# Kernel optimization log

Measured on AMD Instinct MI355X. Metric: run time of the kernel, lower is better.

## Reference

```python
import jax, jax.numpy as jnp
import numpy as np

B, N, K, D = 16, 8192, 20, 64  # batch, points, neighbors, feature dim
LN_EPS = 1e-5


def setup_inputs() -> dict:
    key = jax.random.key(0)
    k1, k2, k3 = jax.random.split(key, 3)
    x = jax.random.normal(k1, (B, N, D), dtype=jnp.float32)
    neighbor_ind = jax.random.randint(k2, (B, N, K), 0, N)
    # torch Linear(2D -> D, bias=False): weight shape (out=D, in=2D), y = feat @ W.T
    W = jax.random.normal(k3, (D, 2 * D), dtype=jnp.float32) * (1.0 / np.sqrt(2 * D))
    gamma = jnp.ones((D,), jnp.float32)
    beta = jnp.zeros((D,), jnp.float32)
    return {"x": x, "neighbor_ind": neighbor_ind, "W": W, "gamma": gamma, "beta": beta}


def reference(x, neighbor_ind, W, gamma, beta):
    # route(): gather neighbor features and build [neighbor - center, center]
    neighbor_x = jax.vmap(lambda xb, ib: xb[ib])(x, neighbor_ind)        # (b, n, k, d)
    center = x[:, :, None, :]                                            # (b, n, 1, d)
    feat = jnp.concatenate(
        [neighbor_x - center, jnp.broadcast_to(center, neighbor_x.shape)], axis=-1
    )                                                                    # (b, n, k, 2d)
    # per-edge Linear (bias=False), then max over k neighbors
    h = jnp.einsum('bnke,oe->bnko', feat, W)                             # (b, n, k, d)
    h = h.max(axis=2)                                                    # (b, n, d)
    # LayerNorm over last dim, then exact GELU
    mu = h.mean(axis=-1, keepdims=True)
    var = jnp.mean((h - mu) ** 2, axis=-1, keepdims=True)
    hn = (h - mu) * jax.lax.rsqrt(var + LN_EPS) * gamma + beta
    return jax.nn.gelu(hn, approximate=False)
```

## Files before the change

### kernel.cpp

```cpp
#include <hip/hip_runtime.h>
#include <math.h>

#define B_ 16
#define N_ 8192
#define K_ 20
#define NPTS (B_ * N_)

typedef __attribute__((ext_vector_type(4))) float f4;
typedef __attribute__((ext_vector_type(8))) short s8;

__device__ __forceinline__ short f2bf(float f) {
    union { float f; unsigned u; } v; v.f = f;
    return (short)((v.u + 0x7FFFu + ((v.u >> 16) & 1u)) >> 16);
}

__device__ __forceinline__ f4 bf4_to_f4(ushort4 v) {
    f4 r;
    r.x = __uint_as_float((unsigned)v.x << 16);
    r.y = __uint_as_float((unsigned)v.y << 16);
    r.z = __uint_as_float((unsigned)v.z << 16);
    r.w = __uint_as_float((unsigned)v.w << 16);
    return r;
}

__global__ __launch_bounds__(256) void prep_kernel(const float* __restrict__ W,
                                                   unsigned short* __restrict__ Wg) {
    const int i = blockIdx.x * 256 + threadIdx.x;
    const int j = i >> 6, d = i & 63;
    const float v = (j < 64) ? W[j * 128 + d]
                             : (W[(j - 64) * 128 + 64 + d] - W[(j - 64) * 128 + d]);
    Wg[i] = (unsigned short)f2bf(v);
}

__global__ __launch_bounds__(256) void proj_kernel(const float* __restrict__ x,
                                                   const unsigned short* __restrict__ Wg,
                                                   unsigned short* __restrict__ Y1,
                                                   float* __restrict__ Bs) {
    __shared__ unsigned short Wl[128 * 72];
    const int t = threadIdx.x;

    for (int i = t; i < 1024; i += 256) {
        int4 v = ((const int4*)Wg)[i];
        *((int4*)((char*)Wl + (i >> 3) * 144 + (i & 7) * 16)) = v;
    }
    __syncthreads();

    const int lane = t & 63;
    const int wv = t >> 6;
    const int m = lane & 15;
    const int q = lane >> 4;
    const int rbase = blockIdx.x * 64 + wv * 16;

    const float* xr = x + (size_t)(rbase + m) * 64 + q * 8;
    f4 x0 = *(const f4*)(xr);
    f4 x1 = *(const f4*)(xr + 4);
    f4 x2 = *(const f4*)(xr + 32);
    f4 x3 = *(const f4*)(xr + 36);
    s8 A0, A1;
    A0[0]=f2bf(x0.x); A0[1]=f2bf(x0.y); A0[2]=f2bf(x0.z); A0[3]=f2bf(x0.w);
    A0[4]=f2bf(x1.x); A0[5]=f2bf(x1.y); A0[6]=f2bf(x1.z); A0[7]=f2bf(x1.w);
    A1[0]=f2bf(x2.x); A1[1]=f2bf(x2.y); A1[2]=f2bf(x2.z); A1[3]=f2bf(x2.w);
    A1[4]=f2bf(x3.x); A1[5]=f2bf(x3.y); A1[6]=f2bf(x3.z); A1[7]=f2bf(x3.w);

    f4 acc[8];
#pragma unroll
    for (int tt = 0; tt < 8; ++tt) acc[tt] = (f4)0.f;

#pragma unroll
    for (int s = 0; s < 2; ++s) {
        const s8 A = s ? A1 : A0;
#pragma unroll
        for (int tt = 0; tt < 8; ++tt) {
            s8 b = *(const s8*)((const char*)Wl + (16 * tt + m) * 144 + s * 64 + q * 16);
            acc[tt] = __builtin_amdgcn_mfma_f32_16x16x32_bf16(A, b, acc[tt], 0, 0, 0);
        }
    }

    const int orow = rbase + q * 4;
#pragma unroll
    for (int tt = 0; tt < 4; ++tt) {
#pragma unroll
        for (int j = 0; j < 4; ++j)
            Y1[(size_t)(orow + j) * 64 + 16 * tt + m] = (unsigned short)f2bf(acc[tt][j]);
    }
#pragma unroll
    for (int tt = 4; tt < 8; ++tt) {
#pragma unroll
        for (int j = 0; j < 4; ++j)
            Bs[(size_t)(orow + j) * 64 + 16 * (tt - 4) + m] = acc[tt][j];
    }
}

__global__ __launch_bounds__(256) void gather_kernel(const unsigned short* __restrict__ Y1,
                                                     const float* __restrict__ Bs,
                                                     const int* __restrict__ ind,
                                                     const float* __restrict__ gamma,
                                                     const float* __restrict__ beta,
                                                     float* __restrict__ out) {
    const int lane = threadIdx.x & 63;
    const int wave = threadIdx.x >> 6;
    const int sub = lane & 15;
    const int q = lane >> 4;
    const int bi = blockIdx.x;
    const int bt = bi & 15;
    const int jj = bi >> 4;
    const int p = bt * N_ + jj * 16 + wave * 4 + q;
    const int bbase = bt * N_ * 64;

    int idxs[K_];
    const int4* ip = (const int4*)&ind[p * K_];
#pragma unroll
    for (int v = 0; v < 5; ++v) {
        int4 iv = ip[v];
        idxs[4 * v + 0] = iv.x; idxs[4 * v + 1] = iv.y;
        idxs[4 * v + 2] = iv.z; idxs[4 * v + 3] = iv.w;
    }

    ushort4 rowv[K_];
#pragma unroll
    for (int k = 0; k < K_; ++k)
        rowv[k] = *(const ushort4*)(Y1 + bbase + idxs[k] * 64 + sub * 4);

    f4 m0 = (f4)(-INFINITY), m1 = (f4)(-INFINITY);
#pragma unroll
    for (int k = 0; k < K_; k += 2) {
        f4 f0 = bf4_to_f4(rowv[k]);
        f4 f1 = bf4_to_f4(rowv[k + 1]);
        m0.x = fmaxf(m0.x, f0.x); m0.y = fmaxf(m0.y, f0.y);
        m0.z = fmaxf(m0.z, f0.z); m0.w = fmaxf(m0.w, f0.w);
        m1.x = fmaxf(m1.x, f1.x); m1.y = fmaxf(m1.y, f1.y);
        m1.z = fmaxf(m1.z, f1.z); m1.w = fmaxf(m1.w, f1.w);
    }
    f4 m;
    m.x = fmaxf(m0.x, m1.x); m.y = fmaxf(m0.y, m1.y);
    m.z = fmaxf(m0.z, m1.z); m.w = fmaxf(m0.w, m1.w);

    f4 base = __builtin_nontemporal_load((const f4*)&Bs[(size_t)p * 64 + sub * 4]);
    f4 h = m + base;

    float s = h.x + h.y + h.z + h.w;
#pragma unroll
    for (int off = 8; off >= 1; off >>= 1) s += __shfl_xor(s, off, 64);
    const float mu = s * (1.0f / 64.0f);
    f4 dv = h - mu;
    float v2 = dv.x * dv.x + dv.y * dv.y + dv.z * dv.z + dv.w * dv.w;
#pragma unroll
    for (int off = 8; off >= 1; off >>= 1) v2 += __shfl_xor(v2, off, 64);
    const float rstd = rsqrtf(v2 * (1.0f / 64.0f) + 1e-5f);

    f4 g4 = *(const f4*)&gamma[sub * 4];
    f4 b4 = *(const f4*)&beta[sub * 4];
    f4 hn = dv * rstd * g4 + b4;

    f4 r;
    r.x = 0.5f * hn.x * (1.0f + erff(hn.x * 0.70710678f));
    r.y = 0.5f * hn.y * (1.0f + erff(hn.y * 0.70710678f));
    r.z = 0.5f * hn.z * (1.0f + erff(hn.z * 0.70710678f));
    r.w = 0.5f * hn.w * (1.0f + erff(hn.w * 0.70710678f));
    __builtin_nontemporal_store(r, (f4*)&out[(size_t)p * 64 + sub * 4]);
}

extern "C" void kernel_launch(void* const* d_in, const int* in_sizes, int n_in,
                              void* d_out, int out_size, void* d_ws, size_t ws_size,
                              hipStream_t stream) {
    const float* x     = (const float*)d_in[0];
    const int*   ind   = (const int*)d_in[1];
    const float* W     = (const float*)d_in[2];
    const float* gamma = (const float*)d_in[3];
    const float* beta  = (const float*)d_in[4];
    float* out = (float*)d_out;

    float* Bs = (float*)d_ws;
    unsigned short* Y1 = (unsigned short*)((char*)d_ws + (size_t)NPTS * 64 * 4);
    unsigned short* Wg = (unsigned short*)((char*)d_ws + (size_t)NPTS * 64 * 6);

    prep_kernel<<<32, 256, 0, stream>>>(W, Wg);
    proj_kernel<<<NPTS / 64, 256, 0, stream>>>(x, Wg, Y1, Bs);
    gather_kernel<<<NPTS / 16, 256, 0, stream>>>(Y1, Bs, ind, gamma, beta, out);
}
```

Before: 139.1 us.

## Store center term in bf16, transpose MFMA for vector stores, widen gather loads

The projection kernel now swaps the MFMA operands so each lane holds four consecutive output channels of one point, which allows packed 8-byte stores instead of scattered 2-byte ones. The center/base term Bs is stored as bf16 instead of fp32, halving its write and read traffic. The gather kernel uses 8 lanes per point with 16-byte loads, so each block covers 32 points and needs fewer shuffle reduction steps. Rounding Bs to bf16 adds error to the pre-LayerNorm values.

```diff
diff --git a/kernel.cpp b/kernel.cpp
--- a/kernel.cpp
+++ b/kernel.cpp
@@ -8,20 +8,15 @@
 
 typedef __attribute__((ext_vector_type(4))) float f4;
 typedef __attribute__((ext_vector_type(8))) short s8;
+typedef __attribute__((ext_vector_type(4))) unsigned int u4;
+typedef __attribute__((ext_vector_type(4))) unsigned short us4;
 
-__device__ __forceinline__ short f2bf(float f) {
+__device__ __forceinline__ unsigned short f2bf(float f) {
     union { float f; unsigned u; } v; v.f = f;
-    return (short)((v.u + 0x7FFFu + ((v.u >> 16) & 1u)) >> 16);
+    return (unsigned short)((v.u + 0x7FFFu + ((v.u >> 16) & 1u)) >> 16);
 }
-
-__device__ __forceinline__ f4 bf4_to_f4(ushort4 v) {
-    f4 r;
-    r.x = __uint_as_float((unsigned)v.x << 16);
-    r.y = __uint_as_float((unsigned)v.y << 16);
-    r.z = __uint_as_float((unsigned)v.z << 16);
-    r.w = __uint_as_float((unsigned)v.w << 16);
-    return r;
-}
+__device__ __forceinline__ float bfhi(unsigned w) { return __uint_as_float(w & 0xFFFF0000u); }
+__device__ __forceinline__ float bflo(unsigned w) { return __uint_as_float(w << 16); }
 
 __global__ __launch_bounds__(256) void prep_kernel(const float* __restrict__ W,
                                                    unsigned short* __restrict__ Wg) {
@@ -29,19 +24,19 @@
     const int j = i >> 6, d = i & 63;
     const float v = (j < 64) ? W[j * 128 + d]
                              : (W[(j - 64) * 128 + 64 + d] - W[(j - 64) * 128 + d]);
-    Wg[i] = (unsigned short)f2bf(v);
+    Wg[i] = f2bf(v);
 }
 
 __global__ __launch_bounds__(256) void proj_kernel(const float* __restrict__ x,
                                                    const unsigned short* __restrict__ Wg,
                                                    unsigned short* __restrict__ Y1,
-                                                   float* __restrict__ Bs) {
+                                                   unsigned short* __restrict__ Bs) {
     __shared__ unsigned short Wl[128 * 72];
     const int t = threadIdx.x;
 
     for (int i = t; i < 1024; i += 256) {
-        int4 v = ((const int4*)Wg)[i];
-        *((int4*)((char*)Wl + (i >> 3) * 144 + (i & 7) * 16)) = v;
+        u4 v = ((const u4*)Wg)[i];
+        *((u4*)((char*)Wl + (i >> 3) * 144 + (i & 7) * 16)) = v;
     }
     __syncthreads();
 
@@ -49,18 +44,18 @@
     const int wv = t >> 6;
     const int m = lane & 15;
     const int q = lane >> 4;
-    const int rbase = blockIdx.x * 64 + wv * 16;
+    const int pbase = blockIdx.x * 64 + wv * 16;
 
-    const float* xr = x + (size_t)(rbase + m) * 64 + q * 8;
+    const float* xr = x + (size_t)(pbase + m) * 64 + q * 8;
     f4 x0 = *(const f4*)(xr);
     f4 x1 = *(const f4*)(xr + 4);
     f4 x2 = *(const f4*)(xr + 32);
     f4 x3 = *(const f4*)(xr + 36);
-    s8 A0, A1;
-    A0[0]=f2bf(x0.x); A0[1]=f2bf(x0.y); A0[2]=f2bf(x0.z); A0[3]=f2bf(x0.w);
-    A0[4]=f2bf(x1.x); A0[5]=f2bf(x1.y); A0[6]=f2bf(x1.z); A0[7]=f2bf(x1.w);
-    A1[0]=f2bf(x2.x); A1[1]=f2bf(x2.y); A1[2]=f2bf(x2.z); A1[3]=f2bf(x2.w);
-    A1[4]=f2bf(x3.x); A1[5]=f2bf(x3.y); A1[6]=f2bf(x3.z); A1[7]=f2bf(x3.w);
+    s8 X0, X1;
+    X0[0]=(short)f2bf(x0.x); X0[1]=(short)f2bf(x0.y); X0[2]=(short)f2bf(x0.z); X0[3]=(short)f2bf(x0.w);
+    X0[4]=(short)f2bf(x1.x); X0[5]=(short)f2bf(x1.y); X0[6]=(short)f2bf(x1.z); X0[7]=(short)f2bf(x1.w);
+    X1[0]=(short)f2bf(x2.x); X1[1]=(short)f2bf(x2.y); X1[2]=(short)f2bf(x2.z); X1[3]=(short)f2bf(x2.w);
+    X1[4]=(short)f2bf(x3.x); X1[5]=(short)f2bf(x3.y); X1[6]=(short)f2bf(x3.z); X1[7]=(short)f2bf(x3.w);
 
     f4 acc[8];
 #pragma unroll
@@ -68,43 +63,45 @@
 
 #pragma unroll
     for (int s = 0; s < 2; ++s) {
-        const s8 A = s ? A1 : A0;
+        const s8 X = s ? X1 : X0;
 #pragma unroll
         for (int tt = 0; tt < 8; ++tt) {
-            s8 b = *(const s8*)((const char*)Wl + (16 * tt + m) * 144 + s * 64 + q * 16);
-            acc[tt] = __builtin_amdgcn_mfma_f32_16x16x32_bf16(A, b, acc[tt], 0, 0, 0);
+            s8 w = *(const s8*)((const char*)Wl + (16 * tt + m) * 144 + s * 64 + q * 16);
+            acc[tt] = __builtin_amdgcn_mfma_f32_16x16x32_bf16(w, X, acc[tt], 0, 0, 0);
         }
     }
 
-    const int orow = rbase + q * 4;
+    const size_t prow = (size_t)(pbase + m) * 64;
 #pragma unroll
     for (int tt = 0; tt < 4; ++tt) {
-#pragma unroll
-        for (int j = 0; j < 4; ++j)
-            Y1[(size_t)(orow + j) * 64 + 16 * tt + m] = (unsigned short)f2bf(acc[tt][j]);
+        us4 u;
+        u.x = f2bf(acc[tt][0]); u.y = f2bf(acc[tt][1]);
+        u.z = f2bf(acc[tt][2]); u.w = f2bf(acc[tt][3]);
+        *(us4*)&Y1[prow + tt * 16 + q * 4] = u;
     }
 #pragma unroll
     for (int tt = 4; tt < 8; ++tt) {
-#pragma unroll
-        for (int j = 0; j < 4; ++j)
-            Bs[(size_t)(orow + j) * 64 + 16 * (tt - 4) + m] = acc[tt][j];
+        us4 u;
+        u.x = f2bf(acc[tt][0]); u.y = f2bf(acc[tt][1]);
+        u.z = f2bf(acc[tt][2]); u.w = f2bf(acc[tt][3]);
+        *(us4*)&Bs[prow + (tt - 4) * 16 + q * 4] = u;
     }
 }
 
 __global__ __launch_bounds__(256) void gather_kernel(const unsigned short* __restrict__ Y1,
-                                                     const float* __restrict__ Bs,
+                                                     const unsigned short* __restrict__ Bs,
                                                      const int* __restrict__ ind,
                                                      const float* __restrict__ gamma,
                                                      const float* __restrict__ beta,
                                                      float* __restrict__ out) {
     const int lane = threadIdx.x & 63;
     const int wave = threadIdx.x >> 6;
-    const int sub = lane & 15;
-    const int q = lane >> 4;
+    const int sub = lane & 7;
+    const int q = lane >> 3;
     const int bi = blockIdx.x;
     const int bt = bi & 15;
     const int jj = bi >> 4;
-    const int p = bt * N_ + jj * 16 + wave * 4 + q;
+    const int p = bt * N_ + jj * 32 + wave * 8 + q;
     const int bbase = bt * N_ * 64;
 
     int idxs[K_];
@@ -116,48 +113,59 @@
         idxs[4 * v + 2] = iv.z; idxs[4 * v + 3] = iv.w;
     }
 
-    ushort4 rowv[K_];
+    f4 ma = (f4)(-INFINITY), mb = (f4)(-INFINITY);
 #pragma unroll
-    for (int k = 0; k < K_; ++k)
-        rowv[k] = *(const ushort4*)(Y1 + bbase + idxs[k] * 64 + sub * 4);
+    for (int r = 0; r < 2; ++r) {
+        u4 rv[10];
+#pragma unroll
+        for (int k = 0; k < 10; ++k)
+            rv[k] = *(const u4*)(Y1 + bbase + idxs[r * 10 + k] * 64 + sub * 8);
+#pragma unroll
+        for (int k = 0; k < 10; ++k) {
+            ma.x = fmaxf(ma.x, bflo(rv[k].x)); ma.y = fmaxf(ma.y, bfhi(rv[k].x));
+            ma.z = fmaxf(ma.z, bflo(rv[k].y)); ma.w = fmaxf(ma.w, bfhi(rv[k].y));
+            mb.x = fmaxf(mb.x, bflo(rv[k].z)); mb.y = fmaxf(mb.y, bfhi(rv[k].z));
+            mb.z = fmaxf(mb.z, bflo(rv[k].w)); mb.w = fmaxf(mb.w, bfhi(rv[k].w));
+        }
+    }
 
-    f4 m0 = (f4)(-INFINITY), m1 = (f4)(-INFINITY);
+    u4 bsv = __builtin_nontemporal_load((const u4*)(Bs + (size_t)p * 64 + sub * 8));
+    f4 ha, hb;
+    ha.x = ma.x + bflo(bsv.x); ha.y = ma.y + bfhi(bsv.x);
+    ha.z = ma.z + bflo(bsv.y); ha.w = ma.w + bfhi(bsv.y);
+    hb.x = mb.x + bflo(bsv.z); hb.y = mb.y + bfhi(bsv.z);
+    hb.z = mb.z + bflo(bsv.w); hb.w = mb.w + bfhi(bsv.w);
+
+    float s = ha.x + ha.y + ha.z + ha.w + hb.x + hb.y + hb.z + hb.w;
 #pragma unroll
-    for (int k = 0; k < K_; k += 2) {
-        f4 f0 = bf4_to_f4(rowv[k]);
-        f4 f1 = bf4_to_f4(rowv[k + 1]);
-        m0.x = fmaxf(m0.x, f0.x); m0.y = fmaxf(m0.y, f0.y);
-        m0.z = fmaxf(m0.z, f0.z); m0.w = fmaxf(m0.w, f0.w);
-        m1.x = fmaxf(m1.x, f1.x); m1.y = fmaxf(m1.y, f1.y);
-        m1.z = fmaxf(m1.z, f1.z); m1.w = fmaxf(m1.w, f1.w);
-    }
-    f4 m;
-    m.x = fmaxf(m0.x, m1.x); m.y = fmaxf(m0.y, m1.y);
-    m.z = fmaxf(m0.z, m1.z); m.w = fmaxf(m0.w, m1.w);
-
-    f4 base = __builtin_nontemporal_load((const f4*)&Bs[(size_t)p * 64 + sub * 4]);
-    f4 h = m + base;
-
-    float s = h.x + h.y + h.z + h.w;
+    for (int off = 4; off >= 1; off >>= 1) s += __shfl_xor(s, off, 64);
+    const float mu = s * (1.0f / 64.0f);
+    f4 da = ha - mu, db = hb - mu;
+    float v2 = da.x * da.x + da.y * da.y + da.z * da.z + da.w * da.w
+             + db.x * db.x + db.y * db.y + db.z * db.z + db.w * db.w;
 #pragma unroll
-    for (int off = 8; off >= 1; off >>= 1) s += __shfl_xor(s, off, 64);
-    const float mu = s * (1.0f / 64.0f);
-    f4 dv = h - mu;
-    float v2 = dv.x * dv.x + dv.y * dv.y + dv.z * dv.z + dv.w * dv.w;
-#pragma unroll
-    for (int off = 8; off >= 1; off >>= 1) v2 += __shfl_xor(v2, off, 64);
+    for (int off = 4; off >= 1; off >>= 1) v2 += __shfl_xor(v2, off, 64);
     const float rstd = rsqrtf(v2 * (1.0f / 64.0f) + 1e-5f);
 
-    f4 g4 = *(const f4*)&gamma[sub * 4];
-    f4 b4 = *(const f4*)&beta[sub * 4];
-    f4 hn = dv * rstd * g4 + b4;
+    const f4 g0 = *(const f4*)&gamma[sub * 8];
+    const f4 g1 = *(const f4*)&gamma[sub * 8 + 4];
+    const f4 b0 = *(const f4*)&beta[sub * 8];
+    const f4 b1 = *(const f4*)&beta[sub * 8 + 4];
+    f4 na = da * rstd * g0 + b0;
+    f4 nb = db * rstd * g1 + b1;
 
-    f4 r;
-    r.x = 0.5f * hn.x * (1.0f + erff(hn.x * 0.70710678f));
-    r.y = 0.5f * hn.y * (1.0f + erff(hn.y * 0.70710678f));
-    r.z = 0.5f * hn.z * (1.0f + erff(hn.z * 0.70710678f));
-    r.w = 0.5f * hn.w * (1.0f + erff(hn.w * 0.70710678f));
-    __builtin_nontemporal_store(r, (f4*)&out[(size_t)p * 64 + sub * 4]);
+    f4 r0, r1;
+    r0.x = 0.5f * na.x * (1.0f + erff(na.x * 0.70710678f));
+    r0.y = 0.5f * na.y * (1.0f + erff(na.y * 0.70710678f));
+    r0.z = 0.5f * na.z * (1.0f + erff(na.z * 0.70710678f));
+    r0.w = 0.5f * na.w * (1.0f + erff(na.w * 0.70710678f));
+    r1.x = 0.5f * nb.x * (1.0f + erff(nb.x * 0.70710678f));
+    r1.y = 0.5f * nb.y * (1.0f + erff(nb.y * 0.70710678f));
+    r1.z = 0.5f * nb.z * (1.0f + erff(nb.z * 0.70710678f));
+    r1.w = 0.5f * nb.w * (1.0f + erff(nb.w * 0.70710678f));
+    float* op = &out[(size_t)p * 64 + sub * 8];
+    __builtin_nontemporal_store(r0, (f4*)op);
+    __builtin_nontemporal_store(r1, (f4*)(op + 4));
 }
 
 extern "C" void kernel_launch(void* const* d_in, const int* in_sizes, int n_in,
@@ -170,11 +178,11 @@
     const float* beta  = (const float*)d_in[4];
     float* out = (float*)d_out;
 
-    float* Bs = (float*)d_ws;
-    unsigned short* Y1 = (unsigned short*)((char*)d_ws + (size_t)NPTS * 64 * 4);
-    unsigned short* Wg = (unsigned short*)((char*)d_ws + (size_t)NPTS * 64 * 6);
+    unsigned short* Bs = (unsigned short*)d_ws;
+    unsigned short* Y1 = Bs + (size_t)NPTS * 64;
+    unsigned short* Wg = Y1 + (size_t)NPTS * 64;
 
     prep_kernel<<<32, 256, 0, stream>>>(W, Wg);
     proj_kernel<<<NPTS / 64, 256, 0, stream>>>(x, Wg, Y1, Bs);
-    gather_kernel<<<NPTS / 16, 256, 0, stream>>>(Y1, Bs, ind, gamma, beta, out);
+    gather_kernel<<<NPTS / 32, 256, 0, stream>>>(Y1, Bs, ind, gamma, beta, out);
 }
```

Measured after the change: 131.7 us. -5.3%, faster.
